# Optimization experiments

Measured on AMD Instinct MI355X. Metric: run time of the kernel, lower is better.

The kernel has to match this reference:

```python
import jax, jax.numpy as jnp
import numpy as np

N = 100_000      # nodes
E = 1_200_000    # edges per graph (avg degree 12)
D = 64           # args.hidden
PROP_STEP = 8
LAM = 1.0
ALP = 1.0 / (LAM + 1.0)   # args.alp <= 0 -> 1/(lam+1)
LAM0 = 1.0
K = 4
LAM_K = 0.5


def setup_inputs() -> dict:
    key = jax.random.key(0)
    k0, k1, k2, k3, k4 = jax.random.split(key, 5)
    x = jax.random.normal(k0, (N, D), dtype=jnp.float32)
    src0 = jax.random.randint(k1, (E,), 0, N, dtype=jnp.int32)
    # ensure every node has in-degree >= 1 (no isolated dst nodes)
    dst0 = jnp.concatenate([jnp.arange(N, dtype=jnp.int32),
                            jax.random.randint(k2, (E - N,), 0, N, dtype=jnp.int32)])
    src1 = jax.random.randint(k3, (E,), 0, N, dtype=jnp.int32)
    dst1 = jnp.concatenate([jnp.arange(N, dtype=jnp.int32),
                            jax.random.randint(k4, (E - N,), 0, N, dtype=jnp.int32)])
    return {"x": x, "src0": src0, "dst0": dst0, "src1": src1, "dst1": dst1}


def _in_degrees(dst):
    # DGL in_degrees(): count of incoming edges per node
    return jax.ops.segment_sum(jnp.ones(dst.shape, jnp.float32), dst, num_segments=N)


def _normalized_AX(src, dst, inv_sqrt_deg, Y):
    # Y <- D^{-1/2} A D^{-1/2} Y  (edge weight w = 1)
    Yn = Y * inv_sqrt_deg                                    # [N, D]
    agg = jax.ops.segment_sum(Yn[src], dst, num_segments=N)  # gather/scatter SpMM
    return agg * inv_sqrt_deg


def reference(x, src0, dst0, src1, dst1):
    deg0 = _in_degrees(dst0)
    deg1 = _in_degrees(dst1)
    # D^{-1/2} with inf -> 0 (as in D_power_X)
    inv0 = jnp.where(deg0 > 0, deg0 ** -0.5, 0.0)[:, None]
    inv1 = jnp.where(deg1 > 0, deg1 ** -0.5, 0.0)[:, None]
    D0 = deg0[:, None]
    D1 = deg1[:, None]
    Y = x
    for _ in range(PROP_STEP):
        nAX0 = _normalized_AX(src0, dst0, inv0, Y)
        nAX1 = _normalized_AX(src1, dst1, inv1, Y)
        Y = Y - ALP * (LAM0 * (Y - x) / (D0 + D1)
                       + LAM * (Y - nAX0)
                       - (LAM_K / K) * (Y - nAX1))
    return Y
```

## Files before the change

kernel.cpp:

```cpp
#include <hip/hip_runtime.h>
#include <hip/hip_fp16.h>

#define NN 100000
#define NE 1200000
#define DIM 64
#define NBINS 391
#define NBE 128
#define CHUNK (NE / NBE)
#define NBLK ((NN + 255) / 256)
#define NPH 7


__global__ void __launch_bounds__(256) bin_count(const int* __restrict__ dst0,
                                                 const int* __restrict__ dst1,
                                                 int* __restrict__ blk_cnt) {
    __shared__ int c[NBINS];
    int t = threadIdx.x;
    for (int i = t; i < NBINS; i += 256) c[i] = 0;
    __syncthreads();
    int lo = blockIdx.x * CHUNK, hi = lo + CHUNK;
    for (int e = lo + t; e < hi; e += 256) {
        atomicAdd(&c[dst0[e] >> 8], 1);
        atomicAdd(&c[dst1[e] >> 8], 1);
    }
    __syncthreads();
    for (int i = t; i < NBINS; i += 256) blk_cnt[blockIdx.x * NBINS + i] = c[i];
}

__global__ void __launch_bounds__(512) bin_scan(const int* __restrict__ blk_cnt,
                                                int* __restrict__ bin_start) {
    __shared__ int tot[512];
    int t = threadIdx.x;
    int s = 0;
    if (t < NBINS)
        for (int b = 0; b < NBE; ++b) s += blk_cnt[b * NBINS + t];
    tot[t] = s;
    __syncthreads();
    for (int off = 1; off < 512; off <<= 1) {
        int v = (t >= off) ? tot[t - off] : 0;
        __syncthreads();
        tot[t] += v;
        __syncthreads();
    }
    if (t <= NBINS) bin_start[t] = tot[t] - s;
}

__global__ void __launch_bounds__(NBE) blk_base_k(const int* __restrict__ blk_cnt,
                                                  const int* __restrict__ bin_start,
                                                  int* __restrict__ blk_base) {
    __shared__ int s[NBE];
    int b = blockIdx.x, t = threadIdx.x;
    int v = blk_cnt[t * NBINS + b];
    s[t] = v;
    __syncthreads();
    for (int off = 1; off < NBE; off <<= 1) {
        int x = (t >= off) ? s[t - off] : 0;
        __syncthreads();
        s[t] += x;
        __syncthreads();
    }
    blk_base[t * NBINS + b] = bin_start[b] + s[t] - v;
}

__global__ void __launch_bounds__(256) bin_permute(const int* __restrict__ src0,
                                                   const int* __restrict__ dst0,
                                                   const int* __restrict__ src1,
                                                   const int* __restrict__ dst1,
                                                   const int* __restrict__ blk_base,
                                                   unsigned int* __restrict__ binned) {
    __shared__ int off[NBINS];
    int t = threadIdx.x;
    for (int i = t; i < NBINS; i += 256) off[i] = blk_base[blockIdx.x * NBINS + i];
    __syncthreads();
    int lo = blockIdx.x * CHUNK, hi = lo + CHUNK;
    for (int e = lo + t; e < hi; e += 256) {
        int s = src0[e], d = dst0[e];
        int p = atomicAdd(&off[d >> 8], 1);
        binned[p] = (unsigned)s | ((unsigned)(d & 255) << 18);
        s = src1[e]; d = dst1[e];
        p = atomicAdd(&off[d >> 8], 1);
        binned[p] = (unsigned)s | (1u << 17) | ((unsigned)(d & 255) << 18);
    }
}

__global__ void __launch_bounds__(256) deg_count(const unsigned int* __restrict__ binned,
                                                 const int* __restrict__ bin_start,
                                                 int* __restrict__ deg0,
                                                 int* __restrict__ deg1) {
    __shared__ int dg[512];
    int b = blockIdx.x, t = threadIdx.x;
    dg[t] = 0; dg[t + 256] = 0;
    __syncthreads();
    int lo = bin_start[b], hi = bin_start[b + 1];
    for (int i = lo + t; i < hi; i += 256) {
        unsigned r = binned[i];
        int dlow = (r >> 18) & 255, g = (r >> 17) & 1;
        atomicAdd(&dg[(dlow << 1) | g], 1);
    }
    __syncthreads();
    int n = b * 256 + t;
    if (n < NN) { deg0[n] = dg[t << 1]; deg1[n] = dg[(t << 1) | 1]; }
}

__global__ void __launch_bounds__(256) scan_l1(const int* __restrict__ deg0,
                                               const int* __restrict__ deg1,
                                               int* __restrict__ rs, int* __restrict__ dp,
                                               int* __restrict__ bs) {
    __shared__ int s0[256];
    int t = threadIdx.x;
    int n = blockIdx.x * 256 + t;
    int a = 0;
    if (n < NN) a = (deg0[n] + deg1[n] + 7) & ~7;
    s0[t] = a;
    __syncthreads();
    for (int off = 1; off < 256; off <<= 1) {
        int x0 = (t >= off) ? s0[t - off] : 0;
        __syncthreads();
        s0[t] += x0;
        __syncthreads();
    }
    if (n < NN) { rs[n] = s0[t] - a; dp[n] = a; }
    if (t == 255) bs[blockIdx.x] = s0[255];
}

__global__ void __launch_bounds__(512) scan_l2(int* __restrict__ bs) {
    __shared__ int s0[512];
    int t = threadIdx.x;
    int a = (t < NBLK) ? bs[t] : 0;
    s0[t] = a;
    __syncthreads();
    for (int off = 1; off < 512; off <<= 1) {
        int x0 = (t >= off) ? s0[t - off] : 0;
        __syncthreads();
        s0[t] += x0;
        __syncthreads();
    }
    if (t < NBLK) bs[t] = s0[t] - a;
}

__global__ void __launch_bounds__(256) scan_l3(int* __restrict__ rs, const int* __restrict__ bs) {
    int n = blockIdx.x * 256 + threadIdx.x;
    if (n < NN) rs[n] += bs[blockIdx.x];
}

__global__ void node_params(const int* __restrict__ deg0, const int* __restrict__ deg1,
                            float2* __restrict__ nsc, float* __restrict__ sc,
                            float* __restrict__ cy) {
    int n = blockIdx.x * blockDim.x + threadIdx.x;
    if (n < NN) {
        int a = deg0[n], b = deg1[n];
        nsc[n] = make_float2((a > 0) ? 0.5f * rsqrtf((float)a) : 0.0f,
                             (b > 0) ? -0.0625f * rsqrtf((float)b) : 0.0f);
        int s = a + b;
        float rD = (s > 0) ? 1.0f / (float)s : 0.0f;
        sc[n] = 0.5625f - 0.5f * rD;
        cy[n] = 0.5f * rD;
    }
}

__global__ void __launch_bounds__(256) csr_scatter(const unsigned int* __restrict__ binned,
                                                   const int* __restrict__ bin_start,
                                                   const int* __restrict__ rs,
                                                   const int* __restrict__ deg0,
                                                   const int* __restrict__ deg1,
                                                   int* __restrict__ es) {
    __shared__ int hist[8 * 256];
    __shared__ int rsl[256];
    __shared__ int degsum[256];
    int b = blockIdx.x, t = threadIdx.x;
    int n = b * 256 + t;
    rsl[t] = (n < NN) ? rs[n] : 0;
    for (int i = t; i < 8 * 256; i += 256) hist[i] = 0;
    __syncthreads();
    int lo = bin_start[b], hi = bin_start[b + 1];
    for (int i = lo + t; i < hi; i += 256) {
        unsigned r = binned[i];
        int ph = (r & 0x1FFFF) >> 14;
        atomicAdd(&hist[ph * 256 + ((r >> 18) & 255)], 1);
    }
    __syncthreads();
    {
        int acc = 0;
        for (int ph = 0; ph < NPH; ++ph) {
            int v = hist[ph * 256 + t];
            hist[ph * 256 + t] = acc;
            acc += v;
        }
        degsum[t] = acc;
    }
    __syncthreads();
    for (int i = lo + t; i < hi; i += 256) {
        unsigned r = binned[i];
        int sN = r & 0x1FFFF, g = (r >> 17) & 1, dlow = (r >> 18) & 255;
        int ph = sN >> 14;
        int p = atomicAdd(&hist[ph * 256 + dlow], 1);
        int dgv = g ? deg1[sN] : deg0[sN];
        es[rsl[dlow] + p] = sN | (g << 17) | (dgv << 18);
    }
    __syncthreads();
    if (n < NN) {
        int base = rsl[t], ds = degsum[t], dpv = (ds + 7) & ~7;
        for (int i = base + ds; i < base + dpv; ++i) es[i] = 0;
    }
}

__global__ void convert_x(const float* __restrict__ X, const float* __restrict__ cy,
                          __half* __restrict__ HA, __half* __restrict__ BX) {
    int i = blockIdx.x * blockDim.x + threadIdx.x;
    if (i < NN * DIM / 4) {
        float4 v = ((const float4*)X)[i];
        float c = cy[i >> 4];
        ushort4 a, b;
        a.x = __half_as_ushort(__float2half(v.x));
        a.y = __half_as_ushort(__float2half(v.y));
        a.z = __half_as_ushort(__float2half(v.z));
        a.w = __half_as_ushort(__float2half(v.w));
        b.x = __half_as_ushort(__float2half(v.x * c));
        b.y = __half_as_ushort(__float2half(v.y * c));
        b.z = __half_as_ushort(__float2half(v.z * c));
        b.w = __half_as_ushort(__float2half(v.w * c));
        ((ushort4*)HA)[i] = a;
        ((ushort4*)BX)[i] = b;
    }
}

__device__ __forceinline__ float4 h4f(ushort4 v) {
    return make_float4(__half2float(__ushort_as_half(v.x)),
                       __half2float(__ushort_as_half(v.y)),
                       __half2float(__ushort_as_half(v.z)),
                       __half2float(__ushort_as_half(v.w)));
}

__global__ void __launch_bounds__(256) step_kernel(
    const __half* __restrict__ Yh, const __half* __restrict__ BX,
    const int* __restrict__ rs, const int* __restrict__ dp,
    const int* __restrict__ es, const float2* __restrict__ nsc,
    const float* __restrict__ sc,
    __half* __restrict__ Yho, float* __restrict__ Ffo)
{
    __shared__ float lut[128];
    for (int i = threadIdx.x; i < 128; i += 256)
        lut[i] = (i == 0) ? 0.0f : rsqrtf((float)i);
    __syncthreads();

    int node = blockIdx.x * 4 + (threadIdx.x >> 6);
    int lane = threadIdx.x & 63;
    int sub  = lane >> 4;
    int fl   = lane & 15;
    int un = __builtin_amdgcn_readfirstlane(node);
    int s  = __builtin_amdgcn_readfirstlane(rs[un]);
    int c  = __builtin_amdgcn_readfirstlane(dp[un]);
    float2 ns = nsc[un];

    float4 acc = make_float4(0.0f, 0.0f, 0.0f, 0.0f);
    int r0 = es[s + sub];
    int r1 = es[s + 4 + sub];
    for (int i = 0; i < c; i += 8) {
        int n0 = es[s + i + 8 + sub];
        int n1 = es[s + i + 12 + sub];
        ushort4 a0 = *(const ushort4*)(Yh + (size_t)(r0 & 0x1FFFF) * DIM + 4 * fl);
        ushort4 a1 = *(const ushort4*)(Yh + (size_t)(r1 & 0x1FFFF) * DIM + 4 * fl);
        float w0 = ((r0 & (1 << 17)) ? ns.y : ns.x) * lut[(unsigned)r0 >> 18];
        float w1 = ((r1 & (1 << 17)) ? ns.y : ns.x) * lut[(unsigned)r1 >> 18];
        float4 f0 = h4f(a0), f1 = h4f(a1);
        acc.x = fmaf(f0.x, w0, acc.x);
        acc.y = fmaf(f0.y, w0, acc.y);
        acc.z = fmaf(f0.z, w0, acc.z);
        acc.w = fmaf(f0.w, w0, acc.w);
        acc.x = fmaf(f1.x, w1, acc.x);
        acc.y = fmaf(f1.y, w1, acc.y);
        acc.z = fmaf(f1.z, w1, acc.z);
        acc.w = fmaf(f1.w, w1, acc.w);
        r0 = n0; r1 = n1;
    }
    acc.x += __shfl_xor(acc.x, 16); acc.x += __shfl_xor(acc.x, 32);
    acc.y += __shfl_xor(acc.y, 16); acc.y += __shfl_xor(acc.y, 32);
    acc.z += __shfl_xor(acc.z, 16); acc.z += __shfl_xor(acc.z, 32);
    acc.w += __shfl_xor(acc.w, 16); acc.w += __shfl_xor(acc.w, 32);

    if (sub == 0) {
        float4 y  = h4f(*(const ushort4*)(Yh + (size_t)un * DIM + 4 * fl));
        float4 bx = h4f(*(const ushort4*)(BX + (size_t)un * DIM + 4 * fl));
        float scl = sc[un];
        float o0 = fmaf(scl, y.x, bx.x) + acc.x;
        float o1 = fmaf(scl, y.y, bx.y) + acc.y;
        float o2 = fmaf(scl, y.z, bx.z) + acc.z;
        float o3 = fmaf(scl, y.w, bx.w) + acc.w;
        if (Ffo) {
            *(float4*)(Ffo + (size_t)un * DIM + 4 * fl) = make_float4(o0, o1, o2, o3);
        } else {
            ushort4 ov;
            ov.x = __half_as_ushort(__float2half(o0));
            ov.y = __half_as_ushort(__float2half(o1));
            ov.z = __half_as_ushort(__float2half(o2));
            ov.w = __half_as_ushort(__float2half(o3));
            *(ushort4*)(Yho + (size_t)un * DIM + 4 * fl) = ov;
        }
    }
}

extern "C" void kernel_launch(void* const* d_in, const int* in_sizes, int n_in,
                              void* d_out, int out_size, void* d_ws, size_t ws_size,
                              hipStream_t stream) {
    const float* x   = (const float*)d_in[0];
    const int* src0  = (const int*)d_in[1];
    const int* dst0  = (const int*)d_in[2];
    const int* src1  = (const int*)d_in[3];
    const int* dst1  = (const int*)d_in[4];
    float* out = (float*)d_out;

    char* ws = (char*)d_ws;
    size_t off = 0;
    auto alloc = [&](size_t bytes) -> void* {
        void* p = ws + off;
        off += (bytes + 255) & ~(size_t)255;
        return p;
    };

    const size_t ES_CAP = (size_t)2 * NE + 8 * NN + 64;

    __half* HA   = (__half*)alloc((size_t)NN * DIM * 2);
    __half* HB   = (__half*)alloc((size_t)NN * DIM * 2);
    __half* BX   = (__half*)alloc((size_t)NN * DIM * 2);
    unsigned int* binned = (unsigned int*)alloc((size_t)2 * NE * 4);
    int*    es   = (int*)alloc(ES_CAP * 4);
    int*    blk_cnt  = (int*)alloc((size_t)NBE * NBINS * 4);
    int*    blk_base = (int*)alloc((size_t)NBE * NBINS * 4);
    int*    bin_st   = (int*)alloc((size_t)(NBINS + 1) * 4);
    int*    deg0 = (int*)alloc((size_t)NN * 4);
    int*    deg1 = (int*)alloc((size_t)NN * 4);
    int*    rs   = (int*)alloc((size_t)NN * 4);
    int*    dp   = (int*)alloc((size_t)NN * 4);
    float2* nsc  = (float2*)alloc((size_t)NN * 8);
    float*  sc   = (float*)alloc((size_t)NN * 4);
    float*  cy   = (float*)alloc((size_t)NN * 4);
    int*    bs   = (int*)alloc((size_t)NBLK * 4);

    const int TB = 256;
    bin_count<<<NBE, 256, 0, stream>>>(dst0, dst1, blk_cnt);
    bin_scan<<<1, 512, 0, stream>>>(blk_cnt, bin_st);
    blk_base_k<<<NBINS, NBE, 0, stream>>>(blk_cnt, bin_st, blk_base);
    bin_permute<<<NBE, 256, 0, stream>>>(src0, dst0, src1, dst1, blk_base, binned);
    deg_count<<<NBINS, 256, 0, stream>>>(binned, bin_st, deg0, deg1);
    scan_l1<<<NBLK, 256, 0, stream>>>(deg0, deg1, rs, dp, bs);
    scan_l2<<<1, 512, 0, stream>>>(bs);
    scan_l3<<<NBLK, 256, 0, stream>>>(rs, bs);
    node_params<<<(NN + TB - 1) / TB, TB, 0, stream>>>(deg0, deg1, nsc, sc, cy);
    csr_scatter<<<NBINS, 256, 0, stream>>>(binned, bin_st, rs, deg0, deg1, es);
    convert_x<<<(NN * DIM / 4 + TB - 1) / TB, TB, 0, stream>>>(x, cy, HA, BX);

    int grid = NN / 4;
    for (int i = 0; i < 8; ++i) {
        const __half* hin = (i & 1) ? HB : HA;
        __half* hout = (i & 1) ? HA : HB;
        float* fout = (i == 7) ? out : nullptr;
        step_kernel<<<grid, TB, 0, stream>>>(hin, BX, rs, dp, es, nsc, sc, hout, fout);
    }
}
```

Before: 501.8 us.

## Precompute fp16 edge weights into CSR entries and software-pipeline gathers

The CSR scatter now computes each edge's full normalized weight (dst scale times source rsqrt degree), rounds it to fp16, and packs it into the upper 15 bits of the edge word alongside the source index. This removes the per-edge LUT lookup, the branch select and the per-node nsc load from the step kernel. The step loop now reads two edge words at once as int2 and prefetches the next pair of feature-row gathers one iteration ahead to overlap memory latency. Dropping the weight's lowest mantissa bit adds a small precision loss, and the prefetch reads further past each node's edge segment, so the edge buffer padding is enlarged.

New measurement: 490.0 us. 2.3% less time.

```diff
diff --git a/kernel.cpp b/kernel.cpp
--- a/kernel.cpp
+++ b/kernel.cpp
@@ -163,13 +163,16 @@
                                                    const int* __restrict__ rs,
                                                    const int* __restrict__ deg0,
                                                    const int* __restrict__ deg1,
+                                                   const float2* __restrict__ nsc,
                                                    int* __restrict__ es) {
     __shared__ int hist[8 * 256];
     __shared__ int rsl[256];
     __shared__ int degsum[256];
+    __shared__ float2 nscl[256];
     int b = blockIdx.x, t = threadIdx.x;
     int n = b * 256 + t;
-    rsl[t] = (n < NN) ? rs[n] : 0;
+    rsl[t]  = (n < NN) ? rs[n] : 0;
+    nscl[t] = (n < NN) ? nsc[n] : make_float2(0.0f, 0.0f);
     for (int i = t; i < 8 * 256; i += 256) hist[i] = 0;
     __syncthreads();
     int lo = bin_start[b], hi = bin_start[b + 1];
@@ -195,7 +198,10 @@
         int ph = sN >> 14;
         int p = atomicAdd(&hist[ph * 256 + dlow], 1);
         int dgv = g ? deg1[sN] : deg0[sN];
-        es[rsl[dlow] + p] = sN | (g << 17) | (dgv << 18);
+        float2 nn = nscl[dlow];
+        float wf = (g ? nn.y : nn.x) * rsqrtf((float)dgv);
+        unsigned u = (unsigned)__half_as_ushort(__float2half(wf));
+        es[rsl[dlow] + p] = (int)((((u + 1u) >> 1) << 17) | (unsigned)sN);
     }
     __syncthreads();
     if (n < NN) {
@@ -231,18 +237,16 @@
                        __half2float(__ushort_as_half(v.w)));
 }
 
+__device__ __forceinline__ float wdec(int r) {
+    return __half2float(__ushort_as_half((unsigned short)(((unsigned)r >> 16) & 0xFFFEu)));
+}
+
 __global__ void __launch_bounds__(256) step_kernel(
     const __half* __restrict__ Yh, const __half* __restrict__ BX,
     const int* __restrict__ rs, const int* __restrict__ dp,
-    const int* __restrict__ es, const float2* __restrict__ nsc,
-    const float* __restrict__ sc,
+    const int* __restrict__ es, const float* __restrict__ sc,
     __half* __restrict__ Yho, float* __restrict__ Ffo)
 {
-    __shared__ float lut[128];
-    for (int i = threadIdx.x; i < 128; i += 256)
-        lut[i] = (i == 0) ? 0.0f : rsqrtf((float)i);
-    __syncthreads();
-
     int node = blockIdx.x * 4 + (threadIdx.x >> 6);
     int lane = threadIdx.x & 63;
     int sub  = lane >> 4;
@@ -250,19 +254,21 @@
     int un = __builtin_amdgcn_readfirstlane(node);
     int s  = __builtin_amdgcn_readfirstlane(rs[un]);
     int c  = __builtin_amdgcn_readfirstlane(dp[un]);
-    float2 ns = nsc[un];
+
+    const int2* ep = (const int2*)(es + s) + sub;
 
     float4 acc = make_float4(0.0f, 0.0f, 0.0f, 0.0f);
-    int r0 = es[s + sub];
-    int r1 = es[s + 4 + sub];
+    int2 rA = ep[0];
+    int2 rB = ep[4];
+    ushort4 gA0 = *(const ushort4*)(Yh + (size_t)(rA.x & 0x1FFFF) * DIM + 4 * fl);
+    ushort4 gA1 = *(const ushort4*)(Yh + (size_t)(rA.y & 0x1FFFF) * DIM + 4 * fl);
     for (int i = 0; i < c; i += 8) {
-        int n0 = es[s + i + 8 + sub];
-        int n1 = es[s + i + 12 + sub];
-        ushort4 a0 = *(const ushort4*)(Yh + (size_t)(r0 & 0x1FFFF) * DIM + 4 * fl);
-        ushort4 a1 = *(const ushort4*)(Yh + (size_t)(r1 & 0x1FFFF) * DIM + 4 * fl);
-        float w0 = ((r0 & (1 << 17)) ? ns.y : ns.x) * lut[(unsigned)r0 >> 18];
-        float w1 = ((r1 & (1 << 17)) ? ns.y : ns.x) * lut[(unsigned)r1 >> 18];
-        float4 f0 = h4f(a0), f1 = h4f(a1);
+        int2 rC = ep[(i >> 1) + 8];
+        ushort4 gB0 = *(const ushort4*)(Yh + (size_t)(rB.x & 0x1FFFF) * DIM + 4 * fl);
+        ushort4 gB1 = *(const ushort4*)(Yh + (size_t)(rB.y & 0x1FFFF) * DIM + 4 * fl);
+        float w0 = wdec(rA.x);
+        float w1 = wdec(rA.y);
+        float4 f0 = h4f(gA0), f1 = h4f(gA1);
         acc.x = fmaf(f0.x, w0, acc.x);
         acc.y = fmaf(f0.y, w0, acc.y);
         acc.z = fmaf(f0.z, w0, acc.z);
@@ -271,7 +277,7 @@
         acc.y = fmaf(f1.y, w1, acc.y);
         acc.z = fmaf(f1.z, w1, acc.z);
         acc.w = fmaf(f1.w, w1, acc.w);
-        r0 = n0; r1 = n1;
+        rA = rB; rB = rC; gA0 = gB0; gA1 = gB1;
     }
     acc.x += __shfl_xor(acc.x, 16); acc.x += __shfl_xor(acc.x, 32);
     acc.y += __shfl_xor(acc.y, 16); acc.y += __shfl_xor(acc.y, 32);
@@ -317,7 +323,7 @@
         return p;
     };
 
-    const size_t ES_CAP = (size_t)2 * NE + 8 * NN + 64;
+    const size_t ES_CAP = (size_t)2 * NE + 8 * NN + 128;
 
     __half* HA   = (__half*)alloc((size_t)NN * DIM * 2);
     __half* HB   = (__half*)alloc((size_t)NN * DIM * 2);
@@ -346,7 +352,7 @@
     scan_l2<<<1, 512, 0, stream>>>(bs);
     scan_l3<<<NBLK, 256, 0, stream>>>(rs, bs);
     node_params<<<(NN + TB - 1) / TB, TB, 0, stream>>>(deg0, deg1, nsc, sc, cy);
-    csr_scatter<<<NBINS, 256, 0, stream>>>(binned, bin_st, rs, deg0, deg1, es);
+    csr_scatter<<<NBINS, 256, 0, stream>>>(binned, bin_st, rs, deg0, deg1, nsc, es);
     convert_x<<<(NN * DIM / 4 + TB - 1) / TB, TB, 0, stream>>>(x, cy, HA, BX);
 
     int grid = NN / 4;
@@ -354,6 +360,6 @@
         const __half* hin = (i & 1) ? HB : HA;
         __half* hout = (i & 1) ? HA : HB;
         float* fout = (i == 7) ? out : nullptr;
-        step_kernel<<<grid, TB, 0, stream>>>(hin, BX, rs, dp, es, nsc, sc, hout, fout);
-    }
-}
+        step_kernel<<<grid, TB, 0, stream>>>(hin, BX, rs, dp, es, sc, hout, fout);
+    }
+}
```
